# Kernel tuning notes

Measured on AMD Instinct MI355X. Metric: run time of the kernel, lower is better.

The kernel has to match this reference:

```python
import jax, jax.numpy as jnp
import numpy as np

B, S, E, D = 4, 2048, 2048, 2048  # batch, seq (<= kvq_dim), embedding_dim, kvq_dim


def setup_inputs() -> dict:
    key = jax.random.key(0)
    kx, kk, kq, kv = jax.random.split(key, 4)
    x = jax.random.normal(kx, (B, S, E), dtype=jnp.float32)
    # torch nn.Linear weights are [out_features, in_features]
    Wk = jax.random.normal(kk, (D, E), dtype=jnp.float32) * 0.02
    Wq = jax.random.normal(kq, (D, E), dtype=jnp.float32) * 0.02
    Wv = jax.random.normal(kv, (D, E), dtype=jnp.float32) * 0.02
    return {"x": x, "Wk": Wk, "Wq": Wq, "Wv": Wv}


def reference(x, Wk, Wq, Wv):
    # Projections (Linear without bias): y = x @ W^T
    K = jnp.einsum("bse,de->bsd", x, Wk)
    Q = jnp.einsum("bse,de->bsd", x, Wq)
    V = jnp.einsum("bse,de->bsd", x, Wv)
    seq = x.shape[1]
    scores = jnp.einsum("bqd,bkd->bqk", Q, K)  # [B, S, S]
    causal = jnp.triu(jnp.ones((seq, seq), dtype=bool), k=1)
    masked = jnp.where(causal[None, :, :], -jnp.inf, scores)
    scale = K.shape[-1] ** 0.5  # -inf / scale stays -inf, matching the torch order
    attn = jax.nn.softmax(masked / scale, axis=-1)
    # dropout: reference evaluated in eval mode (identity)
    return jnp.einsum("bqk,bkd->bqd", attn, V)
```

## Files before the change

### kernel.cpp

```cpp
#include <hip/hip_runtime.h>
#include <hip/hip_bf16.h>
#include <stdint.h>


typedef unsigned short u16;
typedef unsigned int u32;
typedef __bf16 bf16x8 __attribute__((ext_vector_type(8)));
typedef float floatx4 __attribute__((ext_vector_type(4)));

#define DEVI __device__ __forceinline__

constexpr int Bn = 4, Sn = 2048, En = 2048, Dn = 2048;

DEVI u16 f2b(float f) {
  union { float f; u32 u; } v; v.f = f;
  u32 r = v.u + 0x7FFFu + ((v.u >> 16) & 1u);
  return (u16)(r >> 16);
}

DEVI void cp16(const u16* g, u16* l) {
  __builtin_amdgcn_global_load_lds(
      (const __attribute__((address_space(1))) void*)g,
      (__attribute__((address_space(3))) void*)l, 16, 0, 0);
}

__global__ __launch_bounds__(256)
void cvt_kernel(const float* __restrict__ src, u16* __restrict__ dst, int n) {
  int i = (blockIdx.x * 256 + threadIdx.x) * 8;
  if (i >= n) return;
  float4 a = *(const float4*)&src[i];
  float4 b = *(const float4*)&src[i + 4];
  *(ushort4*)&dst[i]     = make_ushort4(f2b(a.x), f2b(a.y), f2b(a.z), f2b(a.w));
  *(ushort4*)&dst[i + 4] = make_ushort4(f2b(b.x), f2b(b.y), f2b(b.z), f2b(b.w));
}

DEVI void gemm8(const u16* __restrict__ A, const u16* __restrict__ Bt,
                int lda, int ldb, int m0, int n0, int kEnd, u16* lds,
                floatx4 acc[8][4]) {
  const int tid = threadIdx.x;
  const int wave = tid >> 6, lane = tid & 63;
  const int wm = (wave >> 2) * 128, wn = (wave & 3) * 64;
  const int quad = lane >> 4, l16 = lane & 15;
  const int swe = (quad ^ ((l16 >> 1) & 3)) * 8;
  const int nkt = kEnd >> 6;

  int dstc[2];
  const u16 *Asp[2], *Bsp[2];
#pragma unroll
  for (int q = 0; q < 2; ++q) {
    int c0 = (q * 8 + wave) * 64;
    int c = c0 + lane;
    int sr = c >> 2;
    int sg = ((c & 3) ^ ((sr >> 1) & 3)) * 8;
    dstc[q] = c0 * 8;
    Asp[q] = A + (size_t)(m0 + sr) * lda + sg;
    Bsp[q] = Bt + (size_t)(n0 + sr) * ldb + sg;
  }
  const int rbA = (wm + l16) * 32 + swe;
  const int rbB = 16384 + (wn + l16) * 32 + swe;

#define STAGE(ktu, isB, sh)                                                  \
  {                                                                          \
    int kc = (ktu) < nkt ? (ktu) : (nkt - 1);  \
    int ks = (kc << 6) + (sh) * 32;                                          \
    int db = (((ktu) & 1) << 15) + (isB) * 16384 + (sh) * 8192;              \
    cp16(((isB) ? Bsp[0] : Asp[0]) + ks, &lds[db + dstc[0]]);                \
    cp16(((isB) ? Bsp[1] : Asp[1]) + ks, &lds[db + dstc[1]]);                \
  }

  STAGE(0, 0, 0); STAGE(0, 1, 0); STAGE(0, 0, 1); STAGE(0, 1, 1);
  STAGE(1, 0, 0); STAGE(1, 1, 0);
  asm volatile("s_waitcnt vmcnt(4)" ::: "memory");
  __builtin_amdgcn_s_barrier();

  for (int m = 0; m < nkt; ++m) {
    const int bofs = (m & 1) << 15;
    bf16x8 bf[4];
#pragma unroll
    for (int p = 0; p < 4; ++p) {
      const int s = p >> 1, cm = p & 1;
      bf16x8 af[4];
      const int abase = bofs + s * 8192 + rbA + cm * 2048;
#pragma unroll
      for (int i = 0; i < 4; ++i) af[i] = *(const bf16x8*)&lds[abase + i * 512];
      if (cm == 0) {
        const int bbase = bofs + s * 8192 + rbB;
#pragma unroll
        for (int j = 0; j < 4; ++j) bf[j] = *(const bf16x8*)&lds[bbase + j * 512];
      }
      if (p == 0)      { STAGE(m + 1, 0, 1); }
      else if (p == 1) { STAGE(m + 1, 1, 1); }
      else if (p == 2) { STAGE(m + 2, 0, 0); }
      else             { STAGE(m + 2, 1, 0); }
      __builtin_amdgcn_s_barrier();
      asm volatile("s_waitcnt lgkmcnt(0)" ::: "memory");
      __builtin_amdgcn_sched_barrier(0);
      __builtin_amdgcn_s_setprio(1);
#pragma unroll
      for (int i = 0; i < 4; ++i)
#pragma unroll
        for (int j = 0; j < 4; ++j)
          acc[cm * 4 + i][j] = __builtin_amdgcn_mfma_f32_16x16x32_bf16(
              af[i], bf[j], acc[cm * 4 + i][j], 0, 0, 0);
      __builtin_amdgcn_s_setprio(0);
      if (p == 3) asm volatile("s_waitcnt vmcnt(4)" ::: "memory");
      __builtin_amdgcn_s_barrier();
    }
  }
#undef STAGE
}

__global__ __launch_bounds__(512, 2)
void proj_kernel(const u16* __restrict__ x, const u16* __restrict__ Wq,
                 const u16* __restrict__ Wk, const u16* __restrict__ Wv,
                 u16* __restrict__ Q, u16* __restrict__ K, u16* __restrict__ Vt) {
  __shared__ __align__(16) u16 lds[65536];
  const int z = blockIdx.z;
  const u16* W = (z == 0) ? Wq : (z == 1) ? Wk : Wv;
  const int m0 = blockIdx.y * 256, n0 = blockIdx.x * 256;
  floatx4 acc[8][4] = {};
  gemm8(x, W, En, En, m0, n0, En, lds, acc);

  const int lane = threadIdx.x & 63, wave = threadIdx.x >> 6;
  const int wm = (wave >> 2) * 128, wn = (wave & 3) * 64;
  const int quad = lane >> 4, l16 = lane & 15;

  if (z < 2) {
    u16* dst = (z == 0) ? Q : K;
#pragma unroll
    for (int mi = 0; mi < 8; ++mi) {
      int t0 = m0 + wm + mi * 16 + quad * 4;
#pragma unroll
      for (int j = 0; j < 4; ++j) {
        int gn = n0 + wn + j * 16 + l16;
#pragma unroll
        for (int r = 0; r < 4; ++r)
          dst[(size_t)(t0 + r) * Dn + gn] = f2b(acc[mi][j][r]);
      }
    }
  } else {
#pragma unroll
    for (int mi = 0; mi < 8; ++mi) {
      int t0 = m0 + wm + mi * 16 + quad * 4;
      int b = t0 >> 11, s0 = t0 & (Sn - 1);
#pragma unroll
      for (int j = 0; j < 4; ++j) {
        int gn = n0 + wn + j * 16 + l16;
        *(ushort4*)&Vt[((size_t)b * Dn + gn) * Sn + s0] =
            make_ushort4(f2b(acc[mi][j][0]), f2b(acc[mi][j][1]),
                         f2b(acc[mi][j][2]), f2b(acc[mi][j][3]));
      }
    }
  }
}

__global__ __launch_bounds__(512, 2)
void scores_kernel(const u16* __restrict__ Q, const u16* __restrict__ K,
                   float* __restrict__ Sc) {
  const int b = blockIdx.z;
  const int m0 = blockIdx.y * 256, n0 = blockIdx.x * 256;
  float* C = Sc + (size_t)b * Sn * Sn;
  if (n0 > m0 + 255) {
    const float4 f = make_float4(-1e30f, -1e30f, -1e30f, -1e30f);
    for (int idx = threadIdx.x; idx < 256 * 64; idx += 512) {
      int r = idx >> 6, c4 = (idx & 63) << 2;
      *(float4*)&C[(size_t)(m0 + r) * Sn + n0 + c4] = f;
    }
    return;
  }
  __shared__ __align__(16) u16 lds[65536];
  floatx4 acc[8][4] = {};
  gemm8(Q + (size_t)b * Sn * Dn, K + (size_t)b * Sn * Dn, Dn, Dn, m0, n0, Dn,
        lds, acc);

  const float inv_scale = 0.022097086912079608f;
  const int lane = threadIdx.x & 63, wave = threadIdx.x >> 6;
  const int wm = (wave >> 2) * 128, wn = (wave & 3) * 64;
  const int quad = lane >> 4, l16 = lane & 15;
#pragma unroll
  for (int mi = 0; mi < 8; ++mi) {
    int gm0 = m0 + wm + mi * 16 + quad * 4;
#pragma unroll
    for (int j = 0; j < 4; ++j) {
      int gn = n0 + wn + j * 16 + l16;
#pragma unroll
      for (int r = 0; r < 4; ++r) {
        float v = acc[mi][j][r] * inv_scale;
        if (gn > gm0 + r) v = -1e30f;
        C[(size_t)(gm0 + r) * Sn + gn] = v;
      }
    }
  }
}

__global__ __launch_bounds__(256)
void softmax_kernel(float* __restrict__ Sc) {
  float* sr = Sc + (size_t)blockIdx.x * Sn;
  const int t = threadIdx.x;
  float4 v0 = ((const float4*)sr)[t];
  float4 v1 = ((const float4*)sr)[t + 256];
  float m = fmaxf(fmaxf(fmaxf(v0.x, v0.y), fmaxf(v0.z, v0.w)),
                  fmaxf(fmaxf(v1.x, v1.y), fmaxf(v1.z, v1.w)));
#pragma unroll
  for (int off = 32; off; off >>= 1) m = fmaxf(m, __shfl_xor(m, off));
  __shared__ float redm[4], reds[4];
  if ((t & 63) == 0) redm[t >> 6] = m;
  __syncthreads();
  m = fmaxf(fmaxf(redm[0], redm[1]), fmaxf(redm[2], redm[3]));

  float e[8];
  e[0] = __expf(v0.x - m); e[1] = __expf(v0.y - m);
  e[2] = __expf(v0.z - m); e[3] = __expf(v0.w - m);
  e[4] = __expf(v1.x - m); e[5] = __expf(v1.y - m);
  e[6] = __expf(v1.z - m); e[7] = __expf(v1.w - m);
  float s = ((e[0] + e[1]) + (e[2] + e[3])) + ((e[4] + e[5]) + (e[6] + e[7]));
#pragma unroll
  for (int off = 32; off; off >>= 1) s += __shfl_xor(s, off);
  if ((t & 63) == 0) reds[t >> 6] = s;
  __syncthreads();
  s = (reds[0] + reds[1]) + (reds[2] + reds[3]);
  float inv = 1.0f / s;

  u16* ar = (u16*)sr;
  *(ushort4*)&ar[t * 4] =
      make_ushort4(f2b(e[0] * inv), f2b(e[1] * inv), f2b(e[2] * inv), f2b(e[3] * inv));
  *(ushort4*)&ar[(t + 256) * 4] =
      make_ushort4(f2b(e[4] * inv), f2b(e[5] * inv), f2b(e[6] * inv), f2b(e[7] * inv));
}

__global__ __launch_bounds__(512, 2)
void pv_kernel(const float* __restrict__ Sc, const u16* __restrict__ Vt,
               float* __restrict__ out) {
  const int b = blockIdx.z;
  const int m0 = blockIdx.y * 256, n0 = blockIdx.x * 256;
  __shared__ __align__(16) u16 lds[65536];
  floatx4 acc[8][4] = {};
  const u16* P = (const u16*)(Sc + (size_t)b * Sn * Sn);
  gemm8(P, Vt + (size_t)b * Dn * Sn, 2 * Sn, Sn, m0, n0, m0 + 256, lds, acc);

  const int lane = threadIdx.x & 63, wave = threadIdx.x >> 6;
  const int wm = (wave >> 2) * 128, wn = (wave & 3) * 64;
  const int quad = lane >> 4, l16 = lane & 15;
  float* ob = out + (size_t)b * Sn * Dn;
#pragma unroll
  for (int mi = 0; mi < 8; ++mi) {
    int gm0 = m0 + wm + mi * 16 + quad * 4;
#pragma unroll
    for (int j = 0; j < 4; ++j) {
      int gn = n0 + wn + j * 16 + l16;
#pragma unroll
      for (int r = 0; r < 4; ++r)
        ob[(size_t)(gm0 + r) * Dn + gn] = acc[mi][j][r];
    }
  }
}

extern "C" void kernel_launch(void* const* d_in, const int* in_sizes, int n_in,
                              void* d_out, int out_size, void* d_ws, size_t ws_size,
                              hipStream_t stream) {
  const float* x  = (const float*)d_in[0];
  const float* Wk = (const float*)d_in[1];
  const float* Wq = (const float*)d_in[2];
  const float* Wv = (const float*)d_in[3];
  float* out = (float*)d_out;

  dim3 blk(256), blk5(512);
  const int nW = Dn * En;
  const size_t MiB = 1ull << 20;

  if (ws_size >= 184 * MiB) {
    u16* Wqb = (u16*)d_ws;
    u16* Wkb = Wqb + (size_t)nW;
    u16* Wvb = Wkb + (size_t)nW;
    u16* xb  = Wvb + (size_t)nW;
    u16* Kall = xb + (size_t)Bn * Sn * En;
    u16* Vtall = Kall + (size_t)Bn * Sn * Dn;
    float* Sc = (float*)(Vtall + (size_t)Bn * Dn * Sn);
    u16* Qall = (u16*)out;

    cvt_kernel<<<nW / 2048, blk, 0, stream>>>(Wq, Wqb, nW);
    cvt_kernel<<<nW / 2048, blk, 0, stream>>>(Wk, Wkb, nW);
    cvt_kernel<<<nW / 2048, blk, 0, stream>>>(Wv, Wvb, nW);
    cvt_kernel<<<(Bn * Sn * En) / 2048, blk, 0, stream>>>(x, xb, Bn * Sn * En);
    proj_kernel<<<dim3(Dn / 256, (Bn * Sn) / 256, 3), blk5, 0, stream>>>(
        xb, Wqb, Wkb, Wvb, Qall, Kall, Vtall);
    scores_kernel<<<dim3(Sn / 256, Sn / 256, Bn), blk5, 0, stream>>>(Qall, Kall, Sc);
    softmax_kernel<<<dim3(Bn * Sn), blk, 0, stream>>>(Sc);
    pv_kernel<<<dim3(Dn / 256, Sn / 256, Bn), blk5, 0, stream>>>(Sc, Vtall, out);
  } else {
    u16* Wqb = (u16*)d_ws;
    u16* Wkb = Wqb + (size_t)nW;
    u16* Wvb = Wkb + (size_t)nW;
    float* Sc = (float*)(Wvb + (size_t)nW);
    u16* xb  = (u16*)Sc;
    u16* Kb  = (u16*)(Sc + (size_t)Sn * Sn);
    u16* Vtb = Kb + (size_t)Sn * Dn;

    cvt_kernel<<<nW / 2048, blk, 0, stream>>>(Wq, Wqb, nW);
    cvt_kernel<<<nW / 2048, blk, 0, stream>>>(Wk, Wkb, nW);
    cvt_kernel<<<nW / 2048, blk, 0, stream>>>(Wv, Wvb, nW);
    for (int b = 0; b < Bn; ++b) {
      const float* xf = x + (size_t)b * Sn * En;
      float* outb = out + (size_t)b * Sn * Dn;
      u16* Qb = (u16*)outb;
      cvt_kernel<<<(Sn * En) / 2048, blk, 0, stream>>>(xf, xb, Sn * En);
      proj_kernel<<<dim3(Dn / 256, Sn / 256, 3), blk5, 0, stream>>>(xb, Wqb, Wkb, Wvb,
                                                                    Qb, Kb, Vtb);
      scores_kernel<<<dim3(Sn / 256, Sn / 256, 1), blk5, 0, stream>>>(Qb, Kb, Sc);
      softmax_kernel<<<dim3(Sn), blk, 0, stream>>>(Sc);
      pv_kernel<<<dim3(Dn / 256, Sn / 256, 1), blk5, 0, stream>>>(Sc, Vtb, outb);
    }
  }
}
```

Before: 491.6 us.

## Restructure GEMM main loop into two half-K phases with fewer barriers

The inner GEMM loop is reworked so that each 64-wide K tile loads all A and B fragments for both 32-wide halves into registers up front, then issues two back-to-back groups of 32 MFMAs. The earlier version used four sub-phases, each with two barriers. The new loop uses two barriers per K tile and places the global->LDS staging between the two LDS read groups. This is meant to cut barrier and synchronisation overhead and give the scheduler longer uninterrupted MFMA runs. The cost is higher register pressure from holding 24 fragment vectors, which could cause spills at 2 blocks per CU with 512 threads.

```diff
diff --git a/kernel.cpp b/kernel.cpp
--- a/kernel.cpp
+++ b/kernel.cpp
@@ -34,7 +34,7 @@
   *(ushort4*)&dst[i + 4] = make_ushort4(f2b(b.x), f2b(b.y), f2b(b.z), f2b(b.w));
 }
 
-DEVI void gemm8(const u16* __restrict__ A, const u16* __restrict__ Bt,
+DEVI void gemmS(const u16* __restrict__ A, const u16* __restrict__ Bt,
                 int lda, int ldb, int m0, int n0, int kEnd, u16* lds,
                 floatx4 acc[8][4]) {
   const int tid = threadIdx.x;
@@ -75,37 +75,43 @@
 
   for (int m = 0; m < nkt; ++m) {
     const int bofs = (m & 1) << 15;
-    bf16x8 bf[4];
-#pragma unroll
-    for (int p = 0; p < 4; ++p) {
-      const int s = p >> 1, cm = p & 1;
-      bf16x8 af[4];
-      const int abase = bofs + s * 8192 + rbA + cm * 2048;
-#pragma unroll
-      for (int i = 0; i < 4; ++i) af[i] = *(const bf16x8*)&lds[abase + i * 512];
-      if (cm == 0) {
-        const int bbase = bofs + s * 8192 + rbB;
-#pragma unroll
-        for (int j = 0; j < 4; ++j) bf[j] = *(const bf16x8*)&lds[bbase + j * 512];
-      }
-      if (p == 0)      { STAGE(m + 1, 0, 1); }
-      else if (p == 1) { STAGE(m + 1, 1, 1); }
-      else if (p == 2) { STAGE(m + 2, 0, 0); }
-      else             { STAGE(m + 2, 1, 0); }
-      __builtin_amdgcn_s_barrier();
-      asm volatile("s_waitcnt lgkmcnt(0)" ::: "memory");
-      __builtin_amdgcn_sched_barrier(0);
-      __builtin_amdgcn_s_setprio(1);
-#pragma unroll
-      for (int i = 0; i < 4; ++i)
-#pragma unroll
-        for (int j = 0; j < 4; ++j)
-          acc[cm * 4 + i][j] = __builtin_amdgcn_mfma_f32_16x16x32_bf16(
-              af[i], bf[j], acc[cm * 4 + i][j], 0, 0, 0);
-      __builtin_amdgcn_s_setprio(0);
-      if (p == 3) asm volatile("s_waitcnt vmcnt(4)" ::: "memory");
-      __builtin_amdgcn_s_barrier();
-    }
+    bf16x8 a0[8], b0[4], a1[8], b1[4];
+    {
+      const int ab = bofs + rbA, bb = bofs + rbB;
+#pragma unroll
+      for (int i = 0; i < 8; ++i) a0[i] = *(const bf16x8*)&lds[ab + i * 512];
+#pragma unroll
+      for (int j = 0; j < 4; ++j) b0[j] = *(const bf16x8*)&lds[bb + j * 512];
+    }
+    STAGE(m + 1, 0, 1); STAGE(m + 1, 1, 1);
+    asm volatile("s_waitcnt lgkmcnt(0)" ::: "memory");
+    __builtin_amdgcn_s_barrier();
+    STAGE(m + 2, 0, 0); STAGE(m + 2, 1, 0);
+    {
+      const int ab = bofs + 8192 + rbA, bb = bofs + 8192 + rbB;
+#pragma unroll
+      for (int i = 0; i < 8; ++i) a1[i] = *(const bf16x8*)&lds[ab + i * 512];
+#pragma unroll
+      for (int j = 0; j < 4; ++j) b1[j] = *(const bf16x8*)&lds[bb + j * 512];
+    }
+    __builtin_amdgcn_sched_barrier(0);
+    __builtin_amdgcn_s_setprio(1);
+#pragma unroll
+    for (int i = 0; i < 8; ++i)
+#pragma unroll
+      for (int j = 0; j < 4; ++j)
+        acc[i][j] = __builtin_amdgcn_mfma_f32_16x16x32_bf16(a0[i], b0[j],
+                                                            acc[i][j], 0, 0, 0);
+    __builtin_amdgcn_sched_barrier(0);
+#pragma unroll
+    for (int i = 0; i < 8; ++i)
+#pragma unroll
+      for (int j = 0; j < 4; ++j)
+        acc[i][j] = __builtin_amdgcn_mfma_f32_16x16x32_bf16(a1[i], b1[j],
+                                                            acc[i][j], 0, 0, 0);
+    __builtin_amdgcn_s_setprio(0);
+    asm volatile("s_waitcnt vmcnt(4)" ::: "memory");
+    __builtin_amdgcn_s_barrier();
   }
 #undef STAGE
 }
@@ -119,7 +125,7 @@
   const u16* W = (z == 0) ? Wq : (z == 1) ? Wk : Wv;
   const int m0 = blockIdx.y * 256, n0 = blockIdx.x * 256;
   floatx4 acc[8][4] = {};
-  gemm8(x, W, En, En, m0, n0, En, lds, acc);
+  gemmS(x, W, En, En, m0, n0, En, lds, acc);
 
   const int lane = threadIdx.x & 63, wave = threadIdx.x >> 6;
   const int wm = (wave >> 2) * 128, wn = (wave & 3) * 64;
@@ -170,7 +176,7 @@
   }
   __shared__ __align__(16) u16 lds[65536];
   floatx4 acc[8][4] = {};
-  gemm8(Q + (size_t)b * Sn * Dn, K + (size_t)b * Sn * Dn, Dn, Dn, m0, n0, Dn,
+  gemmS(Q + (size_t)b * Sn * Dn, K + (size_t)b * Sn * Dn, Dn, Dn, m0, n0, Dn,
         lds, acc);
 
   const float inv_scale = 0.022097086912079608f;
@@ -236,7 +242,7 @@
   __shared__ __align__(16) u16 lds[65536];
   floatx4 acc[8][4] = {};
   const u16* P = (const u16*)(Sc + (size_t)b * Sn * Sn);
-  gemm8(P, Vt + (size_t)b * Dn * Sn, 2 * Sn, Sn, m0, n0, m0 + 256, lds, acc);
+  gemmS(P, Vt + (size_t)b * Dn * Sn, 2 * Sn, Sn, m0, n0, m0 + 256, lds, acc);
 
   const int lane = threadIdx.x & 63, wave = threadIdx.x >> 6;
   const int wm = (wave >> 2) * 128, wn = (wave & 3) * 64;
```

New measurement: 496.1 us. About the same (+0.9%).
